# Kernel optimization log

Measured on AMD Instinct MI355X. Metric: run time of the kernel, lower is better.

## Reference

```python
import jax, jax.numpy as jnp
import numpy as np

N_NODES = 100000
N_EDGES = 1600000
D_IN = 128
HID = 32
HEADS = 4
D_OUT = 40
NEG_SLOPE = 0.2


def edge_softmax(scores, dst, n_nodes):
    # scores: [E, H]; softmax over incoming edges of each destination node
    m = jax.ops.segment_max(scores, dst, num_segments=n_nodes)  # [N, H]
    e = jnp.exp(scores - m[dst])
    s = jax.ops.segment_sum(e, dst, num_segments=n_nodes)  # [N, H]
    return e / s[dst]


def gat_conv(x, src, dst, W, attn_l, attn_r, bias):
    # x: [N, Din]; W: [Din, H*F]; attn_l/attn_r: [H, F]; bias: [H*F]
    n = x.shape[0]
    h = (x @ W).reshape(n, HEADS, HID)          # [N, H, F]
    el = jnp.einsum('nhf,hf->nh', h, attn_l)    # [N, H]
    er = jnp.einsum('nhf,hf->nh', h, attn_r)    # [N, H]
    e = jax.nn.leaky_relu(el[src] + er[dst], NEG_SLOPE)  # [E, H]
    a = edge_softmax(e, dst, n)                 # [E, H]
    msg = h[src] * a[:, :, None]                # [E, H, F]
    out = jax.ops.segment_sum(msg, dst, num_segments=n)  # [N, H, F]
    return out + bias.reshape(HEADS, HID)


def setup_inputs() -> dict:
    key = jax.random.key(0)
    ks = jax.random.split(key, 12)
    x = jax.random.normal(ks[0], (N_NODES, D_IN), dtype=jnp.float32)
    src = jax.random.randint(ks[1], (N_EDGES,), 0, N_NODES, dtype=jnp.int32)
    dst = jax.random.randint(ks[2], (N_EDGES,), 0, N_NODES, dtype=jnp.int32)
    s = 0.05
    W1 = jax.random.normal(ks[3], (D_IN, HEADS * HID), dtype=jnp.float32) * s
    al1 = jax.random.normal(ks[4], (HEADS, HID), dtype=jnp.float32) * s
    ar1 = jax.random.normal(ks[5], (HEADS, HID), dtype=jnp.float32) * s
    b1 = jnp.zeros((HEADS * HID,), dtype=jnp.float32)
    W2 = jax.random.normal(ks[6], (HEADS * HID, HEADS * HID), dtype=jnp.float32) * s
    al2 = jax.random.normal(ks[7], (HEADS, HID), dtype=jnp.float32) * s
    ar2 = jax.random.normal(ks[8], (HEADS, HID), dtype=jnp.float32) * s
    b2 = jnp.zeros((HEADS * HID,), dtype=jnp.float32)
    Wout = jax.random.normal(ks[9], (HEADS * HID, D_OUT), dtype=jnp.float32) * s
    bout = jnp.zeros((D_OUT,), dtype=jnp.float32)
    return {"x": x, "src": src, "dst": dst,
            "W1": W1, "al1": al1, "ar1": ar1, "b1": b1,
            "W2": W2, "al2": al2, "ar2": ar2, "b2": b2,
            "Wout": Wout, "bout": bout}


def reference(x, src, dst, W1, al1, ar1, b1, W2, al2, ar2, b2, Wout, bout):
    n = x.shape[0]
    h = gat_conv(x, src, dst, W1, al1, ar1, b1).reshape(n, -1)  # flatten(1)
    h = jax.nn.elu(h)
    h = gat_conv(h, src, dst, W2, al2, ar2, b2).reshape(n, -1)
    h = jax.nn.elu(h)
    return h @ Wout + bout  # final Linear, flatten(1) is a no-op on 2D
```

## Files before the change

kernel.cpp:

```cpp
#include <hip/hip_runtime.h>
#include <hip/hip_fp16.h>
#include <math.h>

#define N_NODES 100000
#define N_EDGES 1600000
#define NEG_SLOPE 0.2f

#define BKT 256
#define NB ((N_NODES + BKT - 1) / BKT)
#define NC 1024
#define CHUNK ((N_EDGES + NC - 1) / NC)

#define WT_STRIDE 136
#define CS_STRIDE 136

typedef _Float16 f16x2 __attribute__((ext_vector_type(2)));
typedef _Float16 f16x4 __attribute__((ext_vector_type(4)));
typedef float f32x4v __attribute__((ext_vector_type(4)));

#define MFMA16(a, b, c) __builtin_amdgcn_mfma_f32_16x16x16f16(a, b, c, 0, 0, 0)

__device__ __forceinline__ float lrelu(float x) { return x > 0.f ? x : NEG_SLOPE * x; }
__device__ __forceinline__ float eluf(float x)  { return x > 0.f ? x : expm1f(x); }


__global__ __launch_bounds__(256) void p1_hist(const int* __restrict__ dst,
                                               int* __restrict__ H) {
  __shared__ int hist[NB];
  int c = blockIdx.x, t = threadIdx.x;
  for (int i = t; i < NB; i += 256) hist[i] = 0;
  __syncthreads();
  int e0 = c * CHUNK, e1 = min(e0 + CHUNK, N_EDGES);
  for (int e = e0 + t; e < e1; e += 256) atomicAdd(&hist[dst[e] >> 8], 1);
  __syncthreads();
  for (int i = t; i < NB; i += 256) H[i * NC + c] = hist[i];
}

__global__ __launch_bounds__(256) void p2_colscan(int* __restrict__ H,
                                                  int* __restrict__ colTotal) {
  __shared__ int sh[256];
  int b = blockIdx.x, t = threadIdx.x;
  int4 v = *(int4*)&H[b * NC + t * 4];
  int tsum = v.x + v.y + v.z + v.w;
  sh[t] = tsum;
  __syncthreads();
  for (int off = 1; off < 256; off <<= 1) {
    int u = (t >= off) ? sh[t - off] : 0;
    __syncthreads();
    sh[t] += u;
    __syncthreads();
  }
  int excl = sh[t] - tsum;
  int4 o;
  o.x = excl;
  o.y = excl + v.x;
  o.z = o.y + v.y;
  o.w = o.z + v.z;
  *(int4*)&H[b * NC + t * 4] = o;
  if (t == 255) colTotal[b] = sh[255];
}

__global__ __launch_bounds__(512) void p3_bucketscan(const int* __restrict__ colTotal,
                                                     int* __restrict__ bucketBase) {
  __shared__ int sh[512];
  int t = threadIdx.x;
  int v = (t < NB) ? colTotal[t] : 0;
  sh[t] = v;
  __syncthreads();
  for (int off = 1; off < 512; off <<= 1) {
    int u = (t >= off) ? sh[t - off] : 0;
    __syncthreads();
    sh[t] += u;
    __syncthreads();
  }
  if (t < NB) bucketBase[t] = sh[t] - v;
  if (t == NB - 1) bucketBase[NB] = sh[t];
}

__global__ __launch_bounds__(256) void p4_scatter(const int* __restrict__ src,
                                                  const int* __restrict__ dst,
                                                  const int* __restrict__ H,
                                                  const int* __restrict__ bucketBase,
                                                  int* __restrict__ tmp) {
  __shared__ int cur[NB];
  int c = blockIdx.x, t = threadIdx.x;
  for (int i = t; i < NB; i += 256) cur[i] = bucketBase[i] + H[i * NC + c];
  __syncthreads();
  int e0 = c * CHUNK, e1 = min(e0 + CHUNK, N_EDGES);
  for (int e = e0 + t; e < e1; e += 256) {
    int d = dst[e];
    int pos = atomicAdd(&cur[d >> 8], 1);
    tmp[pos] = (src[e] << 8) | (d & 255);
  }
}

__global__ __launch_bounds__(256) void p5_build(const int* __restrict__ tmp,
                                                const int* __restrict__ bucketBase,
                                                int* __restrict__ rowstart,
                                                int* __restrict__ csr_src) {
  __shared__ int hist[256];
  __shared__ int sh[256];
  __shared__ int cur[256];
  int b = blockIdx.x, t = threadIdx.x;
  int ebase = bucketBase[b], eend = bucketBase[b + 1];
  hist[t] = 0;
  __syncthreads();
  for (int e = ebase + t; e < eend; e += 256) atomicAdd(&hist[tmp[e] & 255], 1);
  __syncthreads();
  int v = hist[t];
  sh[t] = v;
  __syncthreads();
  for (int off = 1; off < 256; off <<= 1) {
    int u = (t >= off) ? sh[t - off] : 0;
    __syncthreads();
    sh[t] += u;
    __syncthreads();
  }
  int excl = sh[t] - v;
  int node = b * 256 + t;
  if (node < N_NODES) rowstart[node] = ebase + excl;
  cur[t] = excl;
  __syncthreads();
  for (int e = ebase + t; e < eend; e += 256) {
    int p = tmp[e];
    int pos = ebase + atomicAdd(&cur[p & 255], 1);
    csr_src[pos] = p >> 8;
  }
  if (b == 0 && t == 0) rowstart[N_NODES] = N_EDGES;
}

template <bool FP16IN>
__global__ __launch_bounds__(256) void gemm128_mfma(const void* __restrict__ Av,
                                                    const float* __restrict__ W,
                                                    const float* __restrict__ al,
                                                    const float* __restrict__ ar,
                                                    __half* __restrict__ C,
                                                    float* __restrict__ el,
                                                    float* __restrict__ er, int N) {
  __shared__ _Float16 WtCs[128 * WT_STRIDE];
  __shared__ float als[128], ars[128];
  int tid = threadIdx.x;
  int wv = tid >> 6;
  int l = tid & 63;
  int li = l & 15, lk = l >> 4;
  int rowBase = blockIdx.x * 64;

  if (tid < 128) { als[tid] = al[tid]; ars[tid] = ar[tid]; }

#pragma unroll 4
  for (int i = 0; i < 32; i++) {
    int idx = tid + 256 * i;
    int c = idx & 127, k = (idx >> 7) * 2;
    f16x2 p;
    p[0] = (_Float16)W[k * 128 + c];
    p[1] = (_Float16)W[(k + 1) * 128 + c];
    *(f16x2*)&WtCs[c * WT_STRIDE + k] = p;
  }

  f16x4 afr[8];
  int ra = min(rowBase + wv * 16 + li, N - 1);
  if constexpr (FP16IN) {
    const _Float16* A = (const _Float16*)Av;
#pragma unroll
    for (int ch = 0; ch < 8; ch++)
      afr[ch] = *(const f16x4*)&A[(size_t)ra * 128 + ch * 16 + lk * 4];
  } else {
    const float* A = (const float*)Av;
#pragma unroll
    for (int ch = 0; ch < 8; ch++) {
      float4 v = *(const float4*)&A[(size_t)ra * 128 + ch * 16 + lk * 4];
      f16x4 a;
      a[0] = (_Float16)v.x; a[1] = (_Float16)v.y;
      a[2] = (_Float16)v.z; a[3] = (_Float16)v.w;
      afr[ch] = a;
    }
  }
  __syncthreads();

  f32x4v acc[8];
#pragma unroll
  for (int ct = 0; ct < 8; ct++) acc[ct] = (f32x4v){0.f, 0.f, 0.f, 0.f};

#pragma unroll
  for (int ch = 0; ch < 8; ch++) {
#pragma unroll
    for (int ct = 0; ct < 8; ct++) {
      f16x4 b = *(const f16x4*)&WtCs[(ct * 16 + li) * WT_STRIDE + ch * 16 + lk * 4];
      acc[ct] = MFMA16(afr[ch], b, acc[ct]);
    }
  }

  float alc[8], arc[8];
#pragma unroll
  for (int ct = 0; ct < 8; ct++) {
    alc[ct] = als[ct * 16 + li];
    arc[ct] = ars[ct * 16 + li];
  }
#pragma unroll
  for (int j = 0; j < 4; j++) {
    float el4[4], er4[4];
#pragma unroll
    for (int hh = 0; hh < 4; hh++) {
      el4[hh] = acc[2 * hh][j] * alc[2 * hh] + acc[2 * hh + 1][j] * alc[2 * hh + 1];
      er4[hh] = acc[2 * hh][j] * arc[2 * hh] + acc[2 * hh + 1][j] * arc[2 * hh + 1];
    }
#pragma unroll
    for (int m = 1; m < 16; m <<= 1) {
#pragma unroll
      for (int hh = 0; hh < 4; hh++) {
        el4[hh] += __shfl_xor(el4[hh], m, 64);
        er4[hh] += __shfl_xor(er4[hh], m, 64);
      }
    }
    int row = rowBase + wv * 16 + lk * 4 + j;
    if (li == 0 && row < N) {
      *(float4*)&el[row * 4] = make_float4(el4[0], el4[1], el4[2], el4[3]);
      *(float4*)&er[row * 4] = make_float4(er4[0], er4[1], er4[2], er4[3]);
    }
  }

  __syncthreads();
#pragma unroll
  for (int j = 0; j < 4; j++) {
    int rl = wv * 16 + lk * 4 + j;
#pragma unroll
    for (int ct = 0; ct < 8; ct++)
      WtCs[rl * CS_STRIDE + ct * 16 + li] = (_Float16)acc[ct][j];
  }
  __syncthreads();
  int rrow = tid >> 2, ckk = tid & 3;
  int grow = rowBase + rrow;
  if (grow < N) {
#pragma unroll
    for (int q = 0; q < 4; q++) {
      float4 v = *(float4*)&WtCs[rrow * CS_STRIDE + ckk * 32 + q * 8];
      *(float4*)&C[(size_t)grow * 128 + ckk * 32 + q * 8] = v;
    }
  }
}

__global__ __launch_bounds__(256) void agg_fused(const __half* __restrict__ h,
                                                 const float* __restrict__ el,
                                                 const float* __restrict__ er,
                                                 const int* __restrict__ rowstart,
                                                 const int* __restrict__ csr_src,
                                                 const float* __restrict__ bias,
                                                 __half* __restrict__ out) {
  __shared__ float wlds[16][17][4];
  __shared__ int   ilds[16][17];
  int tid = threadIdx.x;
  int slot = tid >> 4;
  int l = tid & 15;
  int n = blockIdx.x * 16 + slot;
  if (n >= N_NODES) return;
  int base = rowstart[n];
  int deg = rowstart[n + 1] - base;
  int f0 = l * 8;
  int head = l >> 2;
  float acc[8] = {};
  float lsum = 0.f;

  if (deg > 0) {
    float4 erv = *(const float4*)&er[n * 4];

    for (int t0 = 0; t0 < deg; t0 += 16) {
      int e = t0 + l;
      bool act = e < deg;
      int s = act ? csr_src[base + e] : 0;
      float4 elv = *(const float4*)&el[s * 4];
      float w0 = act ? __expf(fminf(lrelu(elv.x + erv.x), 30.f)) : 0.f;
      float w1 = act ? __expf(fminf(lrelu(elv.y + erv.y), 30.f)) : 0.f;
      float w2 = act ? __expf(fminf(lrelu(elv.z + erv.z), 30.f)) : 0.f;
      float w3 = act ? __expf(fminf(lrelu(elv.w + erv.w), 30.f)) : 0.f;
      *(float4*)&wlds[slot][l][0] = make_float4(w0, w1, w2, w3);
      ilds[slot][l] = s;
      __builtin_amdgcn_wave_barrier();

      int nt = min(16, deg - t0);
#pragma unroll 4
      for (int i = 0; i < nt; i++) {
        int si = ilds[slot][i];
        float wi = wlds[slot][i][head];
        lsum += wi;
        float4 raw = *(const float4*)&h[(size_t)si * 128 + f0];
        const __half2* hp = (const __half2*)&raw;
        float2 c0 = __half22float2(hp[0]);
        float2 c1 = __half22float2(hp[1]);
        float2 c2 = __half22float2(hp[2]);
        float2 c3 = __half22float2(hp[3]);
        acc[0] = fmaf(c0.x, wi, acc[0]); acc[1] = fmaf(c0.y, wi, acc[1]);
        acc[2] = fmaf(c1.x, wi, acc[2]); acc[3] = fmaf(c1.y, wi, acc[3]);
        acc[4] = fmaf(c2.x, wi, acc[4]); acc[5] = fmaf(c2.y, wi, acc[5]);
        acc[6] = fmaf(c3.x, wi, acc[6]); acc[7] = fmaf(c3.y, wi, acc[7]);
      }
      __builtin_amdgcn_wave_barrier();
    }
    float rh = 1.f / lsum;
#pragma unroll
    for (int j = 0; j < 8; j++) acc[j] *= rh;
  }
  float4 b0 = *(const float4*)&bias[f0];
  float4 b1 = *(const float4*)&bias[f0 + 4];
  float r0 = eluf(acc[0] + b0.x), r1 = eluf(acc[1] + b0.y);
  float r2 = eluf(acc[2] + b0.z), r3 = eluf(acc[3] + b0.w);
  float r4 = eluf(acc[4] + b1.x), r5 = eluf(acc[5] + b1.y);
  float r6 = eluf(acc[6] + b1.z), r7 = eluf(acc[7] + b1.w);
  __half2 pk[4];
  pk[0] = __float22half2_rn(make_float2(r0, r1));
  pk[1] = __float22half2_rn(make_float2(r2, r3));
  pk[2] = __float22half2_rn(make_float2(r4, r5));
  pk[3] = __float22half2_rn(make_float2(r6, r7));
  *(float4*)&out[(size_t)n * 128 + f0] = *(float4*)pk;
}

__global__ __launch_bounds__(256) void gemm_out_k(const __half* __restrict__ A,
                                                  const float* __restrict__ Wo,
                                                  const float* __restrict__ bo,
                                                  float* __restrict__ C, int N) {
  __shared__ _Float16 WoT[48 * WT_STRIDE];
  int tid = threadIdx.x;
  int wv = tid >> 6;
  int l = tid & 63;
  int li = l & 15, lk = l >> 4;
  int rowBase = blockIdx.x * 64;

#pragma unroll
  for (int i = 0; i < 12; i++) {
    int idx = tid + 256 * i;
    int c = idx >> 6, k2 = (idx & 63) * 2;
    f16x2 p;
    p[0] = (c < 40) ? (_Float16)Wo[k2 * 40 + c] : (_Float16)0.f;
    p[1] = (c < 40) ? (_Float16)Wo[(k2 + 1) * 40 + c] : (_Float16)0.f;
    *(f16x2*)&WoT[c * WT_STRIDE + k2] = p;
  }

  f16x4 afr[8];
  int ra = min(rowBase + wv * 16 + li, N - 1);
  const _Float16* Ah = (const _Float16*)A;
#pragma unroll
  for (int ch = 0; ch < 8; ch++)
    afr[ch] = *(const f16x4*)&Ah[(size_t)ra * 128 + ch * 16 + lk * 4];
  __syncthreads();

  f32x4v acc[3];
#pragma unroll
  for (int ct = 0; ct < 3; ct++) acc[ct] = (f32x4v){0.f, 0.f, 0.f, 0.f};

#pragma unroll
  for (int ch = 0; ch < 8; ch++) {
#pragma unroll
    for (int ct = 0; ct < 3; ct++) {
      f16x4 b = *(const f16x4*)&WoT[(ct * 16 + li) * WT_STRIDE + ch * 16 + lk * 4];
      acc[ct] = MFMA16(afr[ch], b, acc[ct]);
    }
  }

#pragma unroll
  for (int ct = 0; ct < 3; ct++) {
    int col = ct * 16 + li;
    if (col < 40) {
      float bv = bo[col];
#pragma unroll
      for (int j = 0; j < 4; j++) {
        int row = rowBase + wv * 16 + lk * 4 + j;
        if (row < N) C[(size_t)row * 40 + col] = acc[ct][j] + bv;
      }
    }
  }
}

extern "C" void kernel_launch(void* const* d_in, const int* in_sizes, int n_in,
                              void* d_out, int out_size, void* d_ws, size_t ws_size,
                              hipStream_t stream) {
  const float* x    = (const float*)d_in[0];
  const int*   src  = (const int*)d_in[1];
  const int*   dst  = (const int*)d_in[2];
  const float* W1   = (const float*)d_in[3];
  const float* al1  = (const float*)d_in[4];
  const float* ar1  = (const float*)d_in[5];
  const float* b1   = (const float*)d_in[6];
  const float* W2   = (const float*)d_in[7];
  const float* al2  = (const float*)d_in[8];
  const float* ar2  = (const float*)d_in[9];
  const float* b2   = (const float*)d_in[10];
  const float* Wout = (const float*)d_in[11];
  const float* bout = (const float*)d_in[12];
  float* out = (float*)d_out;

  const int N = N_NODES, E = N_EDGES;
  size_t off = 0;
  auto alloc = [&](size_t bytes) {
    void* p = (char*)d_ws + off;
    off += (bytes + 255) & ~(size_t)255;
    return p;
  };
  __half* hh  = (__half*)alloc((size_t)N * 128 * 2);
  __half* o16 = (__half*)alloc((size_t)N * 128 * 2);
  float* el  = (float*)alloc((size_t)N * 4 * 4);
  float* er  = (float*)alloc((size_t)N * 4 * 4);
  int* rowstart   = (int*)alloc((size_t)(N + 1) * 4);
  int* H          = (int*)alloc((size_t)NB * NC * 4);
  int* colTotal   = (int*)alloc((size_t)NB * 4);
  int* bucketBase = (int*)alloc((size_t)(NB + 1) * 4);
  int* tmp        = (int*)alloc((size_t)E * 4);
  int* csr_src    = (int*)alloc((size_t)E * 4);
  (void)ws_size; (void)in_sizes; (void)n_in; (void)out_size;

  p1_hist<<<NC, 256, 0, stream>>>(dst, H);
  p2_colscan<<<NB, 256, 0, stream>>>(H, colTotal);
  p3_bucketscan<<<1, 512, 0, stream>>>(colTotal, bucketBase);
  p4_scatter<<<NC, 256, 0, stream>>>(src, dst, H, bucketBase, tmp);
  p5_build<<<NB, 256, 0, stream>>>(tmp, bucketBase, rowstart, csr_src);

  int gemmGrid = (N + 63) / 64;
  int outGrid  = (N + 63) / 64;
  int aggGrid  = (N + 15) / 16;

  gemm128_mfma<false><<<gemmGrid, 256, 0, stream>>>(x, W1, al1, ar1, hh, el, er, N);
  agg_fused<<<aggGrid, 256, 0, stream>>>(hh, el, er, rowstart, csr_src, b1, o16);

  gemm128_mfma<true><<<gemmGrid, 256, 0, stream>>>(o16, W2, al2, ar2, hh, el, er, N);
  agg_fused<<<aggGrid, 256, 0, stream>>>(hh, el, er, rowstart, csr_src, b2, o16);

  gemm_out_k<<<outGrid, 256, 0, stream>>>(o16, Wout, bout, out, N);
}
```

Measured before the change: 279.0 us.

## Split aggregation feature dimension across two blocks per node group

```diff
diff --git a/kernel.cpp b/kernel.cpp
--- a/kernel.cpp
+++ b/kernel.cpp
@@ -245,19 +245,23 @@
                                                  const int* __restrict__ rowstart,
                                                  const int* __restrict__ csr_src,
                                                  const float* __restrict__ bias,
-                                                 __half* __restrict__ out) {
+                                                 __half* __restrict__ out, int NG) {
   __shared__ float wlds[16][17][4];
   __shared__ int   ilds[16][17];
   int tid = threadIdx.x;
+  int r = blockIdx.x & 7;
+  int half = r >> 2;
+  int ng = (blockIdx.x >> 3) * 4 + (r & 3);
+  if (ng >= NG) return;
   int slot = tid >> 4;
   int l = tid & 15;
-  int n = blockIdx.x * 16 + slot;
+  int n = ng * 16 + slot;
   if (n >= N_NODES) return;
   int base = rowstart[n];
   int deg = rowstart[n + 1] - base;
-  int f0 = l * 8;
-  int head = l >> 2;
-  float acc[8] = {};
+  int f0 = half * 64 + l * 4;
+  int head = (half << 1) | (l >> 3);
+  float acc[4] = {};
   float lsum = 0.f;
 
   if (deg > 0) {
@@ -282,35 +286,26 @@
         int si = ilds[slot][i];
         float wi = wlds[slot][i][head];
         lsum += wi;
-        float4 raw = *(const float4*)&h[(size_t)si * 128 + f0];
+        float2 raw = *(const float2*)&h[(size_t)si * 128 + f0];
         const __half2* hp = (const __half2*)&raw;
         float2 c0 = __half22float2(hp[0]);
         float2 c1 = __half22float2(hp[1]);
-        float2 c2 = __half22float2(hp[2]);
-        float2 c3 = __half22float2(hp[3]);
         acc[0] = fmaf(c0.x, wi, acc[0]); acc[1] = fmaf(c0.y, wi, acc[1]);
         acc[2] = fmaf(c1.x, wi, acc[2]); acc[3] = fmaf(c1.y, wi, acc[3]);
-        acc[4] = fmaf(c2.x, wi, acc[4]); acc[5] = fmaf(c2.y, wi, acc[5]);
-        acc[6] = fmaf(c3.x, wi, acc[6]); acc[7] = fmaf(c3.y, wi, acc[7]);
       }
       __builtin_amdgcn_wave_barrier();
     }
     float rh = 1.f / lsum;
 #pragma unroll
-    for (int j = 0; j < 8; j++) acc[j] *= rh;
+    for (int j = 0; j < 4; j++) acc[j] *= rh;
   }
   float4 b0 = *(const float4*)&bias[f0];
-  float4 b1 = *(const float4*)&bias[f0 + 4];
   float r0 = eluf(acc[0] + b0.x), r1 = eluf(acc[1] + b0.y);
   float r2 = eluf(acc[2] + b0.z), r3 = eluf(acc[3] + b0.w);
-  float r4 = eluf(acc[4] + b1.x), r5 = eluf(acc[5] + b1.y);
-  float r6 = eluf(acc[6] + b1.z), r7 = eluf(acc[7] + b1.w);
-  __half2 pk[4];
+  __half2 pk[2];
   pk[0] = __float22half2_rn(make_float2(r0, r1));
   pk[1] = __float22half2_rn(make_float2(r2, r3));
-  pk[2] = __float22half2_rn(make_float2(r4, r5));
-  pk[3] = __float22half2_rn(make_float2(r6, r7));
-  *(float4*)&out[(size_t)n * 128 + f0] = *(float4*)pk;
+  *(float2*)&out[(size_t)n * 128 + f0] = *(float2*)pk;
 }
 
 __global__ __launch_bounds__(256) void gemm_out_k(const __half* __restrict__ A,
@@ -414,13 +409,14 @@
 
   int gemmGrid = (N + 63) / 64;
   int outGrid  = (N + 63) / 64;
-  int aggGrid  = (N + 15) / 16;
+  int NG = (N + 15) / 16;
+  int aggGrid = ((NG + 3) / 4) * 8;
 
   gemm128_mfma<false><<<gemmGrid, 256, 0, stream>>>(x, W1, al1, ar1, hh, el, er, N);
-  agg_fused<<<aggGrid, 256, 0, stream>>>(hh, el, er, rowstart, csr_src, b1, o16);
+  agg_fused<<<aggGrid, 256, 0, stream>>>(hh, el, er, rowstart, csr_src, b1, o16, NG);
 
   gemm128_mfma<true><<<gemmGrid, 256, 0, stream>>>(o16, W2, al2, ar2, hh, el, er, N);
-  agg_fused<<<aggGrid, 256, 0, stream>>>(hh, el, er, rowstart, csr_src, b2, o16);
+  agg_fused<<<aggGrid, 256, 0, stream>>>(hh, el, er, rowstart, csr_src, b2, o16, NG);
 
   gemm_out_k<<<outGrid, 256, 0, stream>>>(o16, Wout, bout, out, N);
 }
```

New measurement: 284.4 us. About the same (+1.9%).
